# Performance work log

Hardware: AMD Instinct MI355X
Metric: run time of the kernel (lower is better)

## Reference

```python
import jax, jax.numpy as jnp
import numpy as np

FP8_MAX = 448.0  # float8_e4m3fn max
BLOCK = 128


def _quant_blocks_1d(x, bs=BLOCK, eps=1e-12):
    """Block-wise (along last dim) fp8 e4m3 quantization of activations.
    x: (M, K) float32 -> (x_q_f32 (M,K) on fp8 grid, scales (M, K//bs))."""
    M, K = x.shape
    xb = x.reshape(M, K // bs, bs)
    amax = jnp.max(jnp.abs(xb), axis=-1)                     # (M, Kb)
    s = jnp.maximum(amax / FP8_MAX, eps)                     # (M, Kb)
    xq = jnp.clip(xb / s[..., None], -FP8_MAX, FP8_MAX)
    xq = xq.astype(jnp.float8_e4m3fn).astype(jnp.float32)    # round to fp8 grid
    return xq.reshape(M, K), s


def _quant_weight_2d(w, bs=BLOCK, eps=1e-12):
    """2D block-wise fp8 quantization of weight (out, in) -> fp8-grid values + (Nb,Kb) scales."""
    N, K = w.shape
    wb = w.reshape(N // bs, bs, K // bs, bs)
    amax = jnp.max(jnp.abs(wb), axis=(1, 3))                 # (Nb, Kb)
    s = jnp.maximum(amax / FP8_MAX, eps)
    wq = jnp.clip(wb / s[:, None, :, None], -FP8_MAX, FP8_MAX)
    wq = wq.astype(jnp.float8_e4m3fn).astype(jnp.float32)
    return wq.reshape(N, K), s


def setup_inputs() -> dict:
    key = jax.random.key(0)
    kx, kw = jax.random.split(key)
    M, K, N = 4096, 2048, 8192
    x = jax.random.normal(kx, (M, K), dtype=jnp.float32)
    w = jax.random.normal(kw, (N, K), dtype=jnp.float32) * 0.02
    w_q, w_s = _quant_weight_2d(w)  # pre-quantized at "construction" time
    return {"x": x, "w_q": w_q, "w_s": w_s}


def reference(x, w_q, w_s):
    """FP8Linear forward (Triton path math): quantize x block-wise to fp8,
    block-scaled fp8 GEMM against fp8 weight with (Nb,Kb) weight scales.
    Math is identical to dequant-then-GEMM with fp32 accumulation."""
    bs = BLOCK
    M, K = x.shape
    N = w_q.shape[0]
    x_q, x_s = _quant_blocks_1d(x, bs)                        # (M,K), (M,K//bs)
    # dequantize (fold scales back in) — same values the fused kernel computes
    x_deq = (x_q.reshape(M, K // bs, bs) * x_s[..., None]).reshape(M, K)
    w_deq = (w_q.reshape(N // bs, bs, K // bs, bs) * w_s[:, None, :, None]).reshape(N, K)
    out = x_deq @ w_deq.T                                     # (M, N), fp32 accum
    return out
```

## Files before the change

### kernel.cpp

```cpp
#include <hip/hip_runtime.h>
#include <cstdint>
#include <cstddef>

static constexpr int M = 4096, K = 2048, N = 8192;
static constexpr int KBLK = K / 128;

#define GLOBAL_AS __attribute__((address_space(1)))
#define LDS_AS    __attribute__((address_space(3)))

typedef float f32x4 __attribute__((ext_vector_type(4)));
typedef int   i32x4 __attribute__((ext_vector_type(4)));
typedef int   i32x8 __attribute__((ext_vector_type(8)));


__device__ inline float fp8_e4m3_rne(float a) {
    float mag = fminf(fabsf(a), 448.0f);
    float r;
    if (mag < 0.015625f) {
        r = rintf(mag * 512.0f) * (1.0f / 512.0f);
    } else {
        uint32_t u = __float_as_uint(mag);
        u = (u + ((u >> 20) & 1u) + 0x7FFFFu) & 0xFFF00000u;
        r = fminf(__uint_as_float(u), 448.0f);
    }
    return copysignf(r, a);
}


__global__ void quant_x_kernel(const float* __restrict__ x, uint8_t* __restrict__ xq,
                               float* __restrict__ sxT) {
    int task = blockIdx.x * 8 + (threadIdx.x >> 5);
    int sub  = threadIdx.x & 31;
    int row = task >> 4;
    int kb  = task & 15;
    const float* p = x + (size_t)row * K + kb * 128 + sub * 4;
    float4 v = *reinterpret_cast<const float4*>(p);
    float amax = fmaxf(fmaxf(fabsf(v.x), fabsf(v.y)), fmaxf(fabsf(v.z), fabsf(v.w)));
    #pragma unroll
    for (int off = 16; off; off >>= 1) amax = fmaxf(amax, __shfl_xor(amax, off));
    float s = fmaxf(amax / 448.0f, 1e-12f);
    float q0 = fminf(fmaxf(v.x / s, -448.f), 448.f);
    float q1 = fminf(fmaxf(v.y / s, -448.f), 448.f);
    float q2 = fminf(fmaxf(v.z / s, -448.f), 448.f);
    float q3 = fminf(fmaxf(v.w / s, -448.f), 448.f);
    uint32_t pk = __builtin_amdgcn_cvt_pk_fp8_f32(q0, q1, 0, false);
    pk = __builtin_amdgcn_cvt_pk_fp8_f32(q2, q3, pk, true);
    *reinterpret_cast<uint32_t*>(xq + (size_t)row * K + kb * 128 + sub * 4) = pk;
    if (sub == 0) sxT[(size_t)kb * M + row] = s;
}

__global__ void quant_w_kernel(const float* __restrict__ wq, uint8_t* __restrict__ w8) {
    size_t i = ((size_t)blockIdx.x * blockDim.x + threadIdx.x) * 8;
    float4 a = *reinterpret_cast<const float4*>(wq + i);
    float4 b = *reinterpret_cast<const float4*>(wq + i + 4);
    uint32_t lo = __builtin_amdgcn_cvt_pk_fp8_f32(a.x, a.y, 0, false);
    lo = __builtin_amdgcn_cvt_pk_fp8_f32(a.z, a.w, lo, true);
    uint32_t hi = __builtin_amdgcn_cvt_pk_fp8_f32(b.x, b.y, 0, false);
    hi = __builtin_amdgcn_cvt_pk_fp8_f32(b.z, b.w, hi, true);
    uint2 o; o.x = lo; o.y = hi;
    *reinterpret_cast<uint2*>(w8 + i) = o;
}


__device__ __forceinline__ void stageA8(const uint8_t* __restrict__ g,
                                        uint8_t* l, int h, int tid) {
    #pragma unroll
    for (int i = 0; i < 2; ++i) {
        int t2 = tid + i * 512;
        int lr = t2 >> 3;
        int qs = t2 & 7;
        int r  = (lr >> 6) * 128 + h * 64 + (lr & 63);
        int s  = qs ^ (r & 7);
        int ks = ((s & 3) << 1) | (s >> 2);
        __builtin_amdgcn_global_load_lds(
            (const GLOBAL_AS uint32_t*)(g + (size_t)r * K + (ks << 4)),
            (LDS_AS uint32_t*)(l + r * 128 + qs * 16), 16, 0, 0);
    }
}

__device__ __forceinline__ void stageB8(const uint8_t* __restrict__ g,
                                        uint8_t* l, int h, int tid) {
    #pragma unroll
    for (int i = 0; i < 2; ++i) {
        int t2 = tid + i * 512;
        int lr = t2 >> 3;
        int qs = t2 & 7;
        int r  = (lr >> 5) * 64 + h * 32 + (lr & 31);
        int s  = qs ^ (r & 7);
        int ks = ((s & 3) << 1) | (s >> 2);
        __builtin_amdgcn_global_load_lds(
            (const GLOBAL_AS uint32_t*)(g + (size_t)r * K + (ks << 4)),
            (LDS_AS uint32_t*)(l + r * 128 + qs * 16), 16, 0, 0);
    }
}

#define LOAD_AF(MH, AFV, XSV)                                                     \
  _Pragma("unroll")                                                               \
  for (int m = 0; m < 4; ++m) {                                                   \
    int row = wr * 128 + (MH) * 64 + m * 16 + (lane & 15);                        \
    const char* rp = (const char*)lAp + row * 128;                                \
    i32x4 lo = *(const i32x4*)(rp + (((lg)     ^ (row & 7)) << 4));               \
    i32x4 hi = *(const i32x4*)(rp + (((4 | lg) ^ (row & 7)) << 4));               \
    AFV[m] = __builtin_shufflevector(lo, hi, 0, 1, 2, 3, 4, 5, 6, 7);             \
    XSV[m] = sxl[t * 256 + wr * 128 + (MH) * 64 + m * 16 + (lane & 15)];          \
  }

#define LOAD_BF(NH, BFV)                                                          \
  _Pragma("unroll")                                                               \
  for (int n = 0; n < 2; ++n) {                                                   \
    int row = wc * 64 + (NH) * 32 + n * 16 + (lane & 15);                         \
    const char* rp = (const char*)lBp + row * 128;                                \
    i32x4 lo = *(const i32x4*)(rp + (((lg)     ^ (row & 7)) << 4));               \
    i32x4 hi = *(const i32x4*)(rp + (((4 | lg) ^ (row & 7)) << 4));               \
    BFV[n] = __builtin_shufflevector(lo, hi, 0, 1, 2, 3, 4, 5, 6, 7);             \
  }

#define MFMA8(PD, AFV, BFV)                                                       \
  _Pragma("unroll")                                                               \
  for (int m = 0; m < 4; ++m)                                                     \
    _Pragma("unroll")                                                             \
    for (int n = 0; n < 2; ++n)                                                   \
      PD[m][n] = __builtin_amdgcn_mfma_scale_f32_16x16x128_f8f6f4(                \
          BFV[n], AFV[m], zf4, 0, 0, 0, 0x7F7F7F7F, 0, 0x7F7F7F7F);

#define RESC(PD, XSV, MH, NH)                                                     \
  _Pragma("unroll")                                                               \
  for (int m = 0; m < 4; ++m) {                                                   \
    float sm = XSV[m] * wst;                                                      \
    _Pragma("unroll")                                                             \
    for (int n = 0; n < 2; ++n)                                                   \
      acc[(MH) * 4 + m][(NH) * 2 + n] += sm * PD[m][n];                           \
  }

__global__ __launch_bounds__(512, 2) void gemm_kernel(
    const uint8_t* __restrict__ A, const uint8_t* __restrict__ B,
    const float* __restrict__ sxT_g, const float* __restrict__ Ws,
    float* __restrict__ C) {
    __shared__ uint8_t lA[2][256 * 128];
    __shared__ uint8_t lB[2][256 * 128];
    __shared__ float   sxl[KBLK * 256];
    __shared__ float   wsl[32];

    int cpx = gridDim.x >> 3;
    int sw  = (blockIdx.x & 7) * cpx + (blockIdx.x >> 3);
    int tm = sw & 15;
    int tn = sw >> 4;
    int row0 = tm * 256, col0 = tn * 256;

    int tid = threadIdx.x;
    int wid = tid >> 6, lane = tid & 63;
    int lg  = lane >> 4;
    int wr = wid >> 2, wc = wid & 3;

    const uint8_t* Ag = A + (size_t)row0 * K;
    const uint8_t* Bg = B + (size_t)col0 * K;

    f32x4 acc[8][4] = {};
    const f32x4 zf4 = {0.f, 0.f, 0.f, 0.f};

    if (tid < 32)
        __builtin_amdgcn_global_load_lds(
            (const GLOBAL_AS uint32_t*)(Ws + (tn * 2 + (tid >> 4)) * KBLK + (tid & 15)),
            (LDS_AS uint32_t*)(wsl + tid), 4, 0, 0);
    #pragma unroll
    for (int i = 0; i < 2; ++i) {
        int idx = tid + i * 512;
        __builtin_amdgcn_global_load_lds(
            (const GLOBAL_AS uint32_t*)(sxT_g + (size_t)(idx >> 6) * M + row0 + (idx & 63) * 4),
            (LDS_AS uint32_t*)(sxl + idx * 4), 16, 0, 0);
    }
    stageA8(Ag, lA[0], 0, tid);
    stageA8(Ag, lA[0], 1, tid);
    stageB8(Bg, lB[0], 0, tid);
    stageB8(Bg, lB[0], 1, tid);
    __syncthreads();

    for (int t = 0; t < KBLK; ++t) {
        const uint8_t* lAp = lA[t & 1];
        const uint8_t* lBp = lB[t & 1];
        uint8_t* sA = lA[(t + 1) & 1];
        uint8_t* sB = lB[(t + 1) & 1];
        int tn1 = (t + 1 < KBLK) ? (t + 1) : 0;
        const uint8_t* gA = Ag + (size_t)tn1 * 128;
        const uint8_t* gB = Bg + (size_t)tn1 * 128;
        bool stg = (t + 1 < KBLK);
        i32x8 af[4], bfe[2], bfo[2];
        float xs0[4], xs1[4];
        float wst = wsl[(wc >> 1) * KBLK + t];

        LOAD_AF(0, af, xs0);
        LOAD_BF(0, bfe);
        if (stg) {
            stageA8(gA, sA, 0, tid);
            stageA8(gA, sA, 1, tid);
            stageB8(gB, sB, 0, tid);
            stageB8(gB, sB, 1, tid);
        }
        f32x4 P0[4][2]; MFMA8(P0, af, bfe);
        LOAD_BF(1, bfo);
        RESC(P0, xs0, 0, 0);
        f32x4 P1[4][2]; MFMA8(P1, af, bfo);
        LOAD_AF(1, af, xs1);
        RESC(P1, xs0, 0, 1);
        f32x4 P2[4][2]; MFMA8(P2, af, bfo);
        LOAD_BF(0, bfe);
        RESC(P2, xs1, 1, 1);
        f32x4 P3[4][2]; MFMA8(P3, af, bfe);
        RESC(P3, xs1, 1, 0);

        __syncthreads();
    }

    #pragma unroll
    for (int m = 0; m < 8; ++m)
        #pragma unroll
        for (int j = 0; j < 4; ++j) {
            int rr = row0 + wr * 128 + m * 16 + (lane & 15);
            int cc = col0 + wc * 64 + j * 16 + (lane >> 4) * 4;
            *reinterpret_cast<f32x4*>(&C[(size_t)rr * N + cc]) = acc[m][j];
        }
}


__global__ void xs_kernel(const float* __restrict__ x, float* __restrict__ xs) {
    int task = blockIdx.x * 4 + (threadIdx.x >> 6);
    int lane = threadIdx.x & 63;
    int row = task >> 4, kb = task & 15;
    float2 v = *reinterpret_cast<const float2*>(x + (size_t)row * K + kb * 128 + lane * 2);
    float amax = fmaxf(fabsf(v.x), fabsf(v.y));
    #pragma unroll
    for (int off = 32; off; off >>= 1) amax = fmaxf(amax, __shfl_xor(amax, off));
    if (lane == 0) xs[row * KBLK + kb] = fmaxf(amax / 448.0f, 1e-12f);
}

__global__ __launch_bounds__(256) void fallback_gemm(const float* __restrict__ x,
                                                     const float* __restrict__ wq,
                                                     const float* __restrict__ wsc,
                                                     const float* __restrict__ xs,
                                                     float* __restrict__ C) {
    __shared__ float As[64][128];
    __shared__ float Bs[64][128];
    int tm = blockIdx.x % (M / 64), tn = blockIdx.x / (M / 64);
    int row0 = tm * 64, col0 = tn * 64;
    int tid = threadIdx.x;
    int tr = tid >> 4, tc = tid & 15;
    float acc[4][4] = {};
    for (int kb = 0; kb < KBLK; ++kb) {
        int k0 = kb * 128;
        __syncthreads();
        for (int t = tid * 4; t < 64 * 128; t += 256 * 4) {
            int r = t >> 7, c = t & 127;
            float4 va = *reinterpret_cast<const float4*>(x + (size_t)(row0 + r) * K + k0 + c);
            float sa = xs[(row0 + r) * KBLK + kb];
            va.x = fp8_e4m3_rne(va.x / sa) * sa; va.y = fp8_e4m3_rne(va.y / sa) * sa;
            va.z = fp8_e4m3_rne(va.z / sa) * sa; va.w = fp8_e4m3_rne(va.w / sa) * sa;
            *reinterpret_cast<float4*>(&As[r][c]) = va;
            float4 vb = *reinterpret_cast<const float4*>(wq + (size_t)(col0 + r) * K + k0 + c);
            float sb = wsc[((col0 + r) >> 7) * KBLK + kb];
            vb.x *= sb; vb.y *= sb; vb.z *= sb; vb.w *= sb;
            *reinterpret_cast<float4*>(&Bs[r][c]) = vb;
        }
        __syncthreads();
        for (int kk = 0; kk < 128; ++kk) {
            float a[4], b[4];
            #pragma unroll
            for (int i = 0; i < 4; ++i) a[i] = As[tr * 4 + i][kk];
            #pragma unroll
            for (int j = 0; j < 4; ++j) b[j] = Bs[tc * 4 + j][kk];
            #pragma unroll
            for (int i = 0; i < 4; ++i)
                #pragma unroll
                for (int j = 0; j < 4; ++j) acc[i][j] += a[i] * b[j];
        }
    }
    #pragma unroll
    for (int i = 0; i < 4; ++i)
        #pragma unroll
        for (int j = 0; j < 4; ++j)
            C[(size_t)(row0 + tr * 4 + i) * N + col0 + tc * 4 + j] = acc[i][j];
}


extern "C" void kernel_launch(void* const* d_in, const int* in_sizes, int n_in,
                              void* d_out, int out_size, void* d_ws, size_t ws_size,
                              hipStream_t stream) {
    const float* x  = (const float*)d_in[0];
    const float* wq = (const float*)d_in[1];
    const float* ws = (const float*)d_in[2];
    float* out = (float*)d_out;

    size_t need_fast = (size_t)M * K + (size_t)N * K + (size_t)KBLK * M * 4;
    if (ws_size >= need_fast) {
        uint8_t* xq8 = (uint8_t*)d_ws;
        uint8_t* w8  = xq8 + (size_t)M * K;
        float*   sxT = (float*)(w8 + (size_t)N * K);
        quant_x_kernel<<<M * KBLK / 8, 256, 0, stream>>>(x, xq8, sxT);
        quant_w_kernel<<<(int)(((size_t)N * K / 8) / 256), 256, 0, stream>>>(wq, w8);
        gemm_kernel<<<(M / 256) * (N / 256), 512, 0, stream>>>(xq8, w8, sxT, ws, out);
    } else if (ws_size >= (size_t)M * KBLK * 4) {
        float* xs = (float*)d_ws;
        xs_kernel<<<M * KBLK / 4, 256, 0, stream>>>(x, xs);
        fallback_gemm<<<(M / 64) * (N / 64), 256, 0, stream>>>(x, wq, ws, xs, out);
    }
}
```

Before: 116.8 us.

## Split 256x256 GEMM tile across 16 waves with 64x64 per-wave subtiles

Doubles the GEMM workgroup from 512 to 1024 threads while keeping the 256x256 block tile, so each wave owns a 64x64 output subtile instead of 128x64. The per-iteration body drops from four MFMA groups to two, and the staging helpers are merged into a single row-linear loader. The aim is more waves per CU to hide LDS and global latency. The cost is a lower MFMA-to-LDS-read ratio, since each wave re-reads B fragments for half the A rows. The launch bound now limits each thread to roughly 128 VGPRs, which risks spills.

```diff
diff --git a/kernel.cpp b/kernel.cpp
--- a/kernel.cpp
+++ b/kernel.cpp
@@ -62,14 +62,13 @@
 }
 
 
-__device__ __forceinline__ void stageA8(const uint8_t* __restrict__ g,
-                                        uint8_t* l, int h, int tid) {
+__device__ __forceinline__ void stageT(const uint8_t* __restrict__ g,
+                                       uint8_t* l, int tid) {
     #pragma unroll
     for (int i = 0; i < 2; ++i) {
-        int t2 = tid + i * 512;
-        int lr = t2 >> 3;
+        int t2 = tid + i * 1024;
+        int r  = t2 >> 3;
         int qs = t2 & 7;
-        int r  = (lr >> 6) * 128 + h * 64 + (lr & 63);
         int s  = qs ^ (r & 7);
         int ks = ((s & 3) << 1) | (s >> 2);
         __builtin_amdgcn_global_load_lds(
@@ -78,31 +77,15 @@
     }
 }
 
-__device__ __forceinline__ void stageB8(const uint8_t* __restrict__ g,
-                                        uint8_t* l, int h, int tid) {
-    #pragma unroll
-    for (int i = 0; i < 2; ++i) {
-        int t2 = tid + i * 512;
-        int lr = t2 >> 3;
-        int qs = t2 & 7;
-        int r  = (lr >> 5) * 64 + h * 32 + (lr & 31);
-        int s  = qs ^ (r & 7);
-        int ks = ((s & 3) << 1) | (s >> 2);
-        __builtin_amdgcn_global_load_lds(
-            (const GLOBAL_AS uint32_t*)(g + (size_t)r * K + (ks << 4)),
-            (LDS_AS uint32_t*)(l + r * 128 + qs * 16), 16, 0, 0);
-    }
-}
-
-#define LOAD_AF(MH, AFV, XSV)                                                     \
+#define LOAD_AF()                                                                 \
   _Pragma("unroll")                                                               \
   for (int m = 0; m < 4; ++m) {                                                   \
-    int row = wr * 128 + (MH) * 64 + m * 16 + (lane & 15);                        \
+    int row = wr * 64 + m * 16 + (lane & 15);                                     \
     const char* rp = (const char*)lAp + row * 128;                                \
     i32x4 lo = *(const i32x4*)(rp + (((lg)     ^ (row & 7)) << 4));               \
     i32x4 hi = *(const i32x4*)(rp + (((4 | lg) ^ (row & 7)) << 4));               \
-    AFV[m] = __builtin_shufflevector(lo, hi, 0, 1, 2, 3, 4, 5, 6, 7);             \
-    XSV[m] = sxl[t * 256 + wr * 128 + (MH) * 64 + m * 16 + (lane & 15)];          \
+    af[m] = __builtin_shufflevector(lo, hi, 0, 1, 2, 3, 4, 5, 6, 7);              \
+    xs[m] = sxl[t * 256 + wr * 64 + m * 16 + (lane & 15)];                        \
   }
 
 #define LOAD_BF(NH, BFV)                                                          \
@@ -115,24 +98,24 @@
     BFV[n] = __builtin_shufflevector(lo, hi, 0, 1, 2, 3, 4, 5, 6, 7);             \
   }
 
-#define MFMA8(PD, AFV, BFV)                                                       \
+#define MFMA8(PD, BFV)                                                            \
   _Pragma("unroll")                                                               \
   for (int m = 0; m < 4; ++m)                                                     \
     _Pragma("unroll")                                                             \
     for (int n = 0; n < 2; ++n)                                                   \
       PD[m][n] = __builtin_amdgcn_mfma_scale_f32_16x16x128_f8f6f4(                \
-          BFV[n], AFV[m], zf4, 0, 0, 0, 0x7F7F7F7F, 0, 0x7F7F7F7F);
-
-#define RESC(PD, XSV, MH, NH)                                                     \
+          BFV[n], af[m], zf4, 0, 0, 0, 0x7F7F7F7F, 0, 0x7F7F7F7F);
+
+#define RESC(PD, NH)                                                              \
   _Pragma("unroll")                                                               \
   for (int m = 0; m < 4; ++m) {                                                   \
-    float sm = XSV[m] * wst;                                                      \
+    float sm = xs[m] * wst;                                                       \
     _Pragma("unroll")                                                             \
     for (int n = 0; n < 2; ++n)                                                   \
-      acc[(MH) * 4 + m][(NH) * 2 + n] += sm * PD[m][n];                           \
+      acc[m][(NH) * 2 + n] += sm * PD[m][n];                                      \
   }
 
-__global__ __launch_bounds__(512, 2) void gemm_kernel(
+__global__ __launch_bounds__(1024, 4) void gemm_kernel(
     const uint8_t* __restrict__ A, const uint8_t* __restrict__ B,
     const float* __restrict__ sxT_g, const float* __restrict__ Ws,
     float* __restrict__ C) {
@@ -155,24 +138,21 @@
     const uint8_t* Ag = A + (size_t)row0 * K;
     const uint8_t* Bg = B + (size_t)col0 * K;
 
-    f32x4 acc[8][4] = {};
+    f32x4 acc[4][4] = {};
     const f32x4 zf4 = {0.f, 0.f, 0.f, 0.f};
 
     if (tid < 32)
         __builtin_amdgcn_global_load_lds(
             (const GLOBAL_AS uint32_t*)(Ws + (tn * 2 + (tid >> 4)) * KBLK + (tid & 15)),
             (LDS_AS uint32_t*)(wsl + tid), 4, 0, 0);
-    #pragma unroll
-    for (int i = 0; i < 2; ++i) {
-        int idx = tid + i * 512;
+    {
+        int idx = tid;
         __builtin_amdgcn_global_load_lds(
             (const GLOBAL_AS uint32_t*)(sxT_g + (size_t)(idx >> 6) * M + row0 + (idx & 63) * 4),
             (LDS_AS uint32_t*)(sxl + idx * 4), 16, 0, 0);
     }
-    stageA8(Ag, lA[0], 0, tid);
-    stageA8(Ag, lA[0], 1, tid);
-    stageB8(Bg, lB[0], 0, tid);
-    stageB8(Bg, lB[0], 1, tid);
+    stageT(Ag, lA[0], tid);
+    stageT(Bg, lB[0], tid);
     __syncthreads();
 
     for (int t = 0; t < KBLK; ++t) {
@@ -184,38 +164,27 @@
         const uint8_t* gA = Ag + (size_t)tn1 * 128;
         const uint8_t* gB = Bg + (size_t)tn1 * 128;
         bool stg = (t + 1 < KBLK);
-        i32x8 af[4], bfe[2], bfo[2];
-        float xs0[4], xs1[4];
+        i32x8 af[4], bf0[2], bf1[2];
+        float xs[4];
         float wst = wsl[(wc >> 1) * KBLK + t];
 
-        LOAD_AF(0, af, xs0);
-        LOAD_BF(0, bfe);
-        if (stg) {
-            stageA8(gA, sA, 0, tid);
-            stageA8(gA, sA, 1, tid);
-            stageB8(gB, sB, 0, tid);
-            stageB8(gB, sB, 1, tid);
-        }
-        f32x4 P0[4][2]; MFMA8(P0, af, bfe);
-        LOAD_BF(1, bfo);
-        RESC(P0, xs0, 0, 0);
-        f32x4 P1[4][2]; MFMA8(P1, af, bfo);
-        LOAD_AF(1, af, xs1);
-        RESC(P1, xs0, 0, 1);
-        f32x4 P2[4][2]; MFMA8(P2, af, bfo);
-        LOAD_BF(0, bfe);
-        RESC(P2, xs1, 1, 1);
-        f32x4 P3[4][2]; MFMA8(P3, af, bfe);
-        RESC(P3, xs1, 1, 0);
+        LOAD_AF();
+        LOAD_BF(0, bf0);
+        if (stg) { stageT(gA, sA, tid); stageT(gB, sB, tid); }
+        f32x4 P0[4][2]; MFMA8(P0, bf0);
+        LOAD_BF(1, bf1);
+        RESC(P0, 0);
+        f32x4 P1[4][2]; MFMA8(P1, bf1);
+        RESC(P1, 1);
 
         __syncthreads();
     }
 
     #pragma unroll
-    for (int m = 0; m < 8; ++m)
+    for (int m = 0; m < 4; ++m)
         #pragma unroll
         for (int j = 0; j < 4; ++j) {
-            int rr = row0 + wr * 128 + m * 16 + (lane & 15);
+            int rr = row0 + wr * 64 + m * 16 + (lane & 15);
             int cc = col0 + wc * 64 + j * 16 + (lane >> 4) * 4;
             *reinterpret_cast<f32x4*>(&C[(size_t)rr * N + cc]) = acc[m][j];
         }
@@ -296,7 +265,7 @@
         float*   sxT = (float*)(w8 + (size_t)N * K);
         quant_x_kernel<<<M * KBLK / 8, 256, 0, stream>>>(x, xq8, sxT);
         quant_w_kernel<<<(int)(((size_t)N * K / 8) / 256), 256, 0, stream>>>(wq, w8);
-        gemm_kernel<<<(M / 256) * (N / 256), 512, 0, stream>>>(xq8, w8, sxT, ws, out);
+        gemm_kernel<<<(M / 256) * (N / 256), 1024, 0, stream>>>(xq8, w8, sxT, ws, out);
     } else if (ws_size >= (size_t)M * KBLK * 4) {
         float* xs = (float*)d_ws;
         xs_kernel<<<M * KBLK / 4, 256, 0, stream>>>(x, xs);
```

Result: slower. 440.8 us (+277.5%).
